# Performance work log

Measured on AMD Instinct MI355X. Metric: run time of the kernel, lower is better.

## Reference

```python
import jax, jax.numpy as jnp
import numpy as np

N_NODES = 50000
N_EDGES = 800000
IN_FEAT = 128
HIDDEN = 256
OUT = 64


def setup_inputs() -> dict:
    key = jax.random.key(0)
    ks = jax.random.split(key, 8)
    x = jax.random.normal(ks[0], (N_NODES, IN_FEAT), dtype=jnp.float32)
    edge_index = jax.random.randint(ks[1], (2, N_EDGES), 0, N_NODES, dtype=jnp.int64)
    s1 = 1.0 / np.sqrt(IN_FEAT)
    s2 = 1.0 / np.sqrt(HIDDEN)
    W1_l = jax.random.uniform(ks[2], (HIDDEN, IN_FEAT), jnp.float32, -s1, s1)
    W1_r = jax.random.uniform(ks[3], (HIDDEN, IN_FEAT), jnp.float32, -s1, s1)
    b1 = jax.random.uniform(ks[4], (HIDDEN,), jnp.float32, -s1, s1)
    W2_l = jax.random.uniform(ks[5], (OUT, HIDDEN), jnp.float32, -s2, s2)
    W2_r = jax.random.uniform(ks[6], (OUT, HIDDEN), jnp.float32, -s2, s2)
    b2 = jax.random.uniform(ks[7], (OUT,), jnp.float32, -s2, s2)
    return {"x": x, "edge_index": edge_index, "W1_l": W1_l, "W1_r": W1_r,
            "b1": b1, "W2_l": W2_l, "W2_r": W2_r, "b2": b2}


def _sage_conv(x, src, dst, W_l, W_r, b):
    # mean aggregation of source features onto destination nodes
    msgs = x[src]                                                   # [E, F]
    agg = jax.ops.segment_sum(msgs, dst, num_segments=N_NODES)      # [N, F]
    cnt = jax.ops.segment_sum(jnp.ones((src.shape[0], 1), x.dtype), dst,
                              num_segments=N_NODES)                 # [N, 1]
    agg = agg / jnp.maximum(cnt, 1.0)
    # out = lin_l(agg) + lin_r(x); bias only on lin_l (PyG SAGEConv)
    return agg @ W_l.T + b + x @ W_r.T


def reference(x, edge_index, W1_l, W1_r, b1, W2_l, W2_r, b2):
    src, dst = edge_index[0], edge_index[1]
    h = jax.nn.relu(_sage_conv(x, src, dst, W1_l, W1_r, b1))
    # dropout is identity in eval mode
    return _sage_conv(h, src, dst, W2_l, W2_r, b2)
```

## Files before the change

kernel.cpp:

```cpp
#include <hip/hip_runtime.h>
#include <hip/hip_bf16.h>

#define N_NODES 50000
#define N_EDGES 800000
#define IN_FEAT 128
#define HIDDEN  256
#define OUT_F   64
#define M_PAD   50048
#define CONV_NB 1024
#define GATH_NB 2048
#define NGROUPS 12500
#define BSH     7
#define NBUCK   391
#define NCHUNK  256
#define BCAP    4096

typedef __attribute__((ext_vector_type(8))) short short8;
typedef __attribute__((ext_vector_type(4))) float f32x4;

static __device__ __forceinline__ unsigned short f2bf(float f) {
    unsigned u = __float_as_uint(f);
    unsigned r = (u + 0x7fffu + ((u >> 16) & 1u)) >> 16;
    return (unsigned short)r;
}
static __device__ __forceinline__ float bflo(unsigned u) { return __uint_as_float(u << 16); }
static __device__ __forceinline__ float bfhi(unsigned u) { return __uint_as_float(u & 0xffff0000u); }

__global__ __launch_bounds__(256) void prep_k(const float* __restrict__ x,
                                              unsigned int* __restrict__ A1u,
                                              const float* __restrict__ W1l,
                                              const float* __restrict__ W1r,
                                              unsigned int* __restrict__ Wf1,
                                              const float* __restrict__ W2l,
                                              const float* __restrict__ W2r,
                                              unsigned int* __restrict__ Wf2,
                                              int* __restrict__ gcur) {
    int b = blockIdx.x, t = threadIdx.x;
    if (b < CONV_NB) {
        const int T = CONV_NB * 256;
        const float4* X4 = (const float4*)x;
        for (int i = b * 256 + t; i < N_NODES * 32; i += T) {
            int n = i >> 5, p4 = i & 31;
            float4 v = X4[i];
            unsigned lo = (unsigned)f2bf(v.x) | ((unsigned)f2bf(v.y) << 16);
            unsigned hi = (unsigned)f2bf(v.z) | ((unsigned)f2bf(v.w) << 16);
            unsigned int* dstp = A1u + (size_t)n * 128 + 64 + p4 * 2;
            dstp[0] = lo; dstp[1] = hi;
        }
    } else if (b < CONV_NB + 128) {
        int i = (b - CONV_NB) * 256 + t;
        int s = i * 2;
        int j = s & 7, lane = (s >> 3) & 63, nt = (s >> 9) & 15, ks = s >> 13;
        int n = nt * 16 + (lane & 15);
        int k = ks * 32 + ((lane >> 4) << 3) + j;
        float v0, v1;
        if (k < 128) { v0 = W1l[n * 128 + k];       v1 = W1l[n * 128 + k + 1]; }
        else         { v0 = W1r[n * 128 + k - 128]; v1 = W1r[n * 128 + k - 127]; }
        Wf1[i] = (unsigned)f2bf(v0) | ((unsigned)f2bf(v1) << 16);
    } else if (b < CONV_NB + 128 + 64) {
        int i = (b - CONV_NB - 128) * 256 + t;
        int s = i * 2;
        int j = s & 7, lane = (s >> 3) & 63, nt = (s >> 9) & 7, ks = s >> 12;
        int n = nt * 16 + (lane & 15);
        int k = ks * 32 + ((lane >> 4) << 3) + j;
        float v0, v1;
        if (n < 64) { v0 = W2l[n * 256 + k];        v1 = W2l[n * 256 + k + 1]; }
        else        { v0 = W2r[(n - 64) * 256 + k]; v1 = W2r[(n - 64) * 256 + k + 1]; }
        Wf2[i] = (unsigned)f2bf(v0) | ((unsigned)f2bf(v1) << 16);
    } else {
        for (int i = t; i < NBUCK; i += 256) gcur[i] = 0;
    }
}

__global__ __launch_bounds__(256) void reorder2_k(const int* __restrict__ dst,
                                                  const int* __restrict__ src,
                                                  int* __restrict__ gcur,
                                                  int2* __restrict__ ebuf) {
    __shared__ int hist[NBUCK];
    __shared__ int cur[NBUCK];
    int b = blockIdx.x, t = threadIdx.x;
    for (int i = t; i < NBUCK; i += 256) hist[i] = 0;
    __syncthreads();
    for (int e = b * 256 + t; e < N_EDGES; e += NCHUNK * 256)
        atomicAdd(&hist[dst[e] >> BSH], 1);
    __syncthreads();
    for (int i = t; i < NBUCK; i += 256) {
        int h = hist[i];
        cur[i] = (h > 0) ? atomicAdd(&gcur[i], h) : 0;
    }
    __syncthreads();
    for (int e = b * 256 + t; e < N_EDGES; e += NCHUNK * 256) {
        int d = dst[e], sv = src[e];
        int q = d >> BSH;
        int pos = atomicAdd(&cur[q], 1);
        if (pos < BCAP) ebuf[(size_t)q * BCAP + pos] = make_int2(sv, d);
    }
}

__global__ __launch_bounds__(256) void bucketcsr_k(const int2* __restrict__ ebuf,
                                                   const int* __restrict__ gcur,
                                                   int* __restrict__ rowptr,
                                                   int* __restrict__ degv,
                                                   int* __restrict__ eids) {
    __shared__ int2 ed[BCAP];
    __shared__ int cnt[128];
    __shared__ int s[256];
    __shared__ int cur[128];
    int b = blockIdx.x, t = threadIdx.x;
    int e0 = b * BCAP;
    int m = gcur[b]; if (m > BCAP) m = BCAP;
    int d0 = b << BSH;
    if (t < 128) cnt[t] = 0;
    for (int i = t; i < m; i += 256) ed[i] = ebuf[e0 + i];
    __syncthreads();
    for (int i = t; i < m; i += 256) atomicAdd(&cnt[ed[i].y - d0], 1);
    __syncthreads();
    s[t] = (t < 128) ? cnt[t] : 0;
    __syncthreads();
    for (int off = 1; off < 256; off <<= 1) {
        int add = (t >= off) ? s[t - off] : 0;
        __syncthreads();
        s[t] += add;
        __syncthreads();
    }
    if (t < 128) {
        int excl = s[t] - cnt[t];
        cur[t] = excl;
        int node = d0 + t;
        if (node < N_NODES) { rowptr[node] = e0 + excl; degv[node] = cnt[t]; }
    }
    __syncthreads();
    for (int i = t; i < m; i += 256) {
        int pos = atomicAdd(&cur[ed[i].y - d0], 1);
        eids[e0 + pos] = ed[i].x;
    }
}

__global__ __launch_bounds__(256) void gather1_k(const unsigned int* __restrict__ Au,
                                                 const int* __restrict__ eids,
                                                 const int* __restrict__ rowptr,
                                                 const int* __restrict__ degv,
                                                 unsigned int* __restrict__ Aw) {
    int w = threadIdx.x >> 6, lane = threadIdx.x & 63;
    int eg = lane >> 4, cq = lane & 15;
    for (int g = blockIdx.x; g < NGROUPS; g += GATH_NB) {
        int node = g * 4 + w;
        int b = rowptr[node], e = b + degv[node];
        float a0 = 0.f, a1 = 0.f, a2 = 0.f, a3 = 0.f, a4 = 0.f, a5 = 0.f, a6 = 0.f, a7 = 0.f;
        int i = b + eg;
        for (; i + 12 < e; i += 16) {
            int s0 = eids[i], s1 = eids[i + 4], s2 = eids[i + 8], s3 = eids[i + 12];
            uint4 v0 = ((const uint4*)(Au + (size_t)s0 * 128 + 64))[cq];
            uint4 v1 = ((const uint4*)(Au + (size_t)s1 * 128 + 64))[cq];
            uint4 v2 = ((const uint4*)(Au + (size_t)s2 * 128 + 64))[cq];
            uint4 v3 = ((const uint4*)(Au + (size_t)s3 * 128 + 64))[cq];
            a0 += bflo(v0.x) + bflo(v1.x) + bflo(v2.x) + bflo(v3.x);
            a1 += bfhi(v0.x) + bfhi(v1.x) + bfhi(v2.x) + bfhi(v3.x);
            a2 += bflo(v0.y) + bflo(v1.y) + bflo(v2.y) + bflo(v3.y);
            a3 += bfhi(v0.y) + bfhi(v1.y) + bfhi(v2.y) + bfhi(v3.y);
            a4 += bflo(v0.z) + bflo(v1.z) + bflo(v2.z) + bflo(v3.z);
            a5 += bfhi(v0.z) + bfhi(v1.z) + bfhi(v2.z) + bfhi(v3.z);
            a6 += bflo(v0.w) + bflo(v1.w) + bflo(v2.w) + bflo(v3.w);
            a7 += bfhi(v0.w) + bfhi(v1.w) + bfhi(v2.w) + bfhi(v3.w);
        }
        for (; i < e; i += 4) {
            int s = eids[i];
            uint4 v = ((const uint4*)(Au + (size_t)s * 128 + 64))[cq];
            a0 += bflo(v.x); a1 += bfhi(v.x);
            a2 += bflo(v.y); a3 += bfhi(v.y);
            a4 += bflo(v.z); a5 += bfhi(v.z);
            a6 += bflo(v.w); a7 += bfhi(v.w);
        }
#pragma unroll
        for (int m = 16; m <= 32; m <<= 1) {
            a0 += __shfl_xor(a0, m); a1 += __shfl_xor(a1, m);
            a2 += __shfl_xor(a2, m); a3 += __shfl_xor(a3, m);
            a4 += __shfl_xor(a4, m); a5 += __shfl_xor(a5, m);
            a6 += __shfl_xor(a6, m); a7 += __shfl_xor(a7, m);
        }
        if (eg == 0) {
            int deg = e - b; if (deg < 1) deg = 1;
            float inv = 1.f / (float)deg;
            uint4 r;
            r.x = (unsigned)f2bf(a0 * inv) | ((unsigned)f2bf(a1 * inv) << 16);
            r.y = (unsigned)f2bf(a2 * inv) | ((unsigned)f2bf(a3 * inv) << 16);
            r.z = (unsigned)f2bf(a4 * inv) | ((unsigned)f2bf(a5 * inv) << 16);
            r.w = (unsigned)f2bf(a6 * inv) | ((unsigned)f2bf(a7 * inv) << 16);
            ((uint4*)(Aw + (size_t)node * 128))[cq] = r;
        }
    }
}

__global__ __launch_bounds__(256) void mfma_gemm1_k(
        const unsigned short* __restrict__ A, const unsigned short* __restrict__ Wf,
        const float* __restrict__ b1, unsigned short* __restrict__ h) {
    int wv = threadIdx.x >> 6, lane = threadIdx.x & 63;
    int rowh = wv >> 1, colh = wv & 1;
    int m0 = blockIdx.x * 64 + rowh * 32;
    int row = lane & 15, kg = lane >> 4;
    const short8* Wf8 = (const short8*)Wf;

    short8 af[2][8];
#pragma unroll
    for (int mt = 0; mt < 2; mt++) {
        const short8* ar = (const short8*)(A + (size_t)(m0 + mt * 16 + row) * 256 + kg * 8);
#pragma unroll
        for (int ks = 0; ks < 8; ks++) af[mt][ks] = ar[ks * 4];
    }
    f32x4 acc[2][8];
#pragma unroll
    for (int mt = 0; mt < 2; mt++)
#pragma unroll
        for (int nt = 0; nt < 8; nt++) acc[mt][nt] = (f32x4)(0.f);

#pragma unroll
    for (int ks = 0; ks < 8; ks++) {
        short8 bf[8];
#pragma unroll
        for (int nt = 0; nt < 8; nt++)
            bf[nt] = Wf8[(ks * 16 + colh * 8 + nt) * 64 + lane];
#pragma unroll
        for (int nt = 0; nt < 8; nt++) {
#pragma unroll
            for (int mt = 0; mt < 2; mt++)
                acc[mt][nt] = __builtin_amdgcn_mfma_f32_16x16x32_bf16(af[mt][ks], bf[nt],
                                                                      acc[mt][nt], 0, 0, 0);
        }
    }

#pragma unroll
    for (int mt = 0; mt < 2; mt++) {
        int r0 = m0 + mt * 16 + kg * 4;
#pragma unroll
        for (int nt = 0; nt < 8; nt++) {
            int c = colh * 128 + nt * 16 + row;
            float bias = b1[c];
#pragma unroll
            for (int i = 0; i < 4; i++) {
                float v = acc[mt][nt][i] + bias;
                v = v > 0.f ? v : 0.f;
                h[(size_t)(r0 + i) * 256 + c] = f2bf(v);
            }
        }
    }
}

__global__ __launch_bounds__(256) void mfma_gemm2_k(
        const unsigned short* __restrict__ A, const unsigned short* __restrict__ Wf,
        const float* __restrict__ b2, unsigned short* __restrict__ y,
        float* __restrict__ out) {
    int wv = threadIdx.x >> 6, lane = threadIdx.x & 63;
    int m0 = blockIdx.x * 128 + wv * 32;
    int row = lane & 15, kg = lane >> 4;
    const short8* Wf8 = (const short8*)Wf;

    short8 af[2][8];
#pragma unroll
    for (int mt = 0; mt < 2; mt++) {
        const short8* ar = (const short8*)(A + (size_t)(m0 + mt * 16 + row) * 256 + kg * 8);
#pragma unroll
        for (int ks = 0; ks < 8; ks++) af[mt][ks] = ar[ks * 4];
    }
    f32x4 acc[2][8];
#pragma unroll
    for (int mt = 0; mt < 2; mt++)
#pragma unroll
        for (int nt = 0; nt < 8; nt++) acc[mt][nt] = (f32x4)(0.f);

#pragma unroll
    for (int ks = 0; ks < 8; ks++) {
        short8 bf[8];
#pragma unroll
        for (int nt = 0; nt < 8; nt++)
            bf[nt] = Wf8[(ks * 8 + nt) * 64 + lane];
#pragma unroll
        for (int nt = 0; nt < 8; nt++) {
#pragma unroll
            for (int mt = 0; mt < 2; mt++)
                acc[mt][nt] = __builtin_amdgcn_mfma_f32_16x16x32_bf16(af[mt][ks], bf[nt],
                                                                      acc[mt][nt], 0, 0, 0);
        }
    }

#pragma unroll
    for (int mt = 0; mt < 2; mt++) {
        int r0 = m0 + mt * 16 + kg * 4;
#pragma unroll
        for (int nt = 0; nt < 8; nt++) {
            int c = nt * 16 + row;
#pragma unroll
            for (int i = 0; i < 4; i++) {
                int rr = r0 + i;
                if (nt < 4) {
                    y[(size_t)rr * OUT_F + c] = f2bf(acc[mt][nt][i]);
                } else if (rr < N_NODES) {
                    out[(size_t)rr * OUT_F + (c - 64)] = acc[mt][nt][i] + b2[c - 64];
                }
            }
        }
    }
}

__global__ __launch_bounds__(256) void gather2_k(const unsigned int* __restrict__ yu,
                                                 const int* __restrict__ eids,
                                                 const int* __restrict__ rowptr,
                                                 const int* __restrict__ degv,
                                                 float* __restrict__ out) {
    int w = threadIdx.x >> 6, lane = threadIdx.x & 63;
    int eg = lane >> 3, cq = lane & 7;
    for (int g = blockIdx.x; g < NGROUPS; g += GATH_NB) {
        int node = g * 4 + w;
        int b = rowptr[node], e = b + degv[node];
        float a0 = 0.f, a1 = 0.f, a2 = 0.f, a3 = 0.f, a4 = 0.f, a5 = 0.f, a6 = 0.f, a7 = 0.f;
        int i = b + eg;
        for (; i + 8 < e; i += 16) {
            int s0 = eids[i], s1 = eids[i + 8];
            uint4 v0 = ((const uint4*)(yu + (size_t)s0 * 32))[cq];
            uint4 v1 = ((const uint4*)(yu + (size_t)s1 * 32))[cq];
            a0 += bflo(v0.x) + bflo(v1.x); a1 += bfhi(v0.x) + bfhi(v1.x);
            a2 += bflo(v0.y) + bflo(v1.y); a3 += bfhi(v0.y) + bfhi(v1.y);
            a4 += bflo(v0.z) + bflo(v1.z); a5 += bfhi(v0.z) + bfhi(v1.z);
            a6 += bflo(v0.w) + bflo(v1.w); a7 += bfhi(v0.w) + bfhi(v1.w);
        }
        for (; i < e; i += 8) {
            int s = eids[i];
            uint4 v = ((const uint4*)(yu + (size_t)s * 32))[cq];
            a0 += bflo(v.x); a1 += bfhi(v.x);
            a2 += bflo(v.y); a3 += bfhi(v.y);
            a4 += bflo(v.z); a5 += bfhi(v.z);
            a6 += bflo(v.w); a7 += bfhi(v.w);
        }
#pragma unroll
        for (int m = 8; m <= 32; m <<= 1) {
            a0 += __shfl_xor(a0, m); a1 += __shfl_xor(a1, m);
            a2 += __shfl_xor(a2, m); a3 += __shfl_xor(a3, m);
            a4 += __shfl_xor(a4, m); a5 += __shfl_xor(a5, m);
            a6 += __shfl_xor(a6, m); a7 += __shfl_xor(a7, m);
        }
        if (eg == 0) {
            int deg = e - b; if (deg < 1) deg = 1;
            float inv = 1.f / (float)deg;
            float4* p = (float4*)(out + (size_t)node * OUT_F + cq * 8);
            float4 c0 = p[0], c1 = p[1];
            c0.x += a0 * inv; c0.y += a1 * inv; c0.z += a2 * inv; c0.w += a3 * inv;
            c1.x += a4 * inv; c1.y += a5 * inv; c1.z += a6 * inv; c1.w += a7 * inv;
            p[0] = c0; p[1] = c1;
        }
    }
}

extern "C" void kernel_launch(void* const* d_in, const int* in_sizes, int n_in,
                              void* d_out, int out_size, void* d_ws, size_t ws_size,
                              hipStream_t stream) {
    const float* x    = (const float*)d_in[0];
    const int*   eidx = (const int*)d_in[1];
    const float* W1l  = (const float*)d_in[2];
    const float* W1r  = (const float*)d_in[3];
    const float* b1   = (const float*)d_in[4];
    const float* W2l  = (const float*)d_in[5];
    const float* W2r  = (const float*)d_in[6];
    const float* b2   = (const float*)d_in[7];
    float* out = (float*)d_out;

    const int* src = eidx;
    const int* dst = eidx + N_EDGES;

    unsigned short* A1   = (unsigned short*)d_ws;
    unsigned short* hbuf = A1 + (size_t)M_PAD * 256;
    unsigned short* ybuf = hbuf + (size_t)M_PAD * 256;
    unsigned short* W1f  = ybuf + (size_t)M_PAD * OUT_F;
    unsigned short* W2f  = W1f + 65536;
    int2* ebuf  = (int2*)(W2f + 32768);
    int* eids   = (int*)(ebuf + (size_t)NBUCK * BCAP);
    int* rowptr = eids + (size_t)NBUCK * BCAP;
    int* degv   = rowptr + N_NODES;
    int* gcur   = degv + N_NODES;

    prep_k<<<CONV_NB + 128 + 64 + 1, 256, 0, stream>>>(x, (unsigned int*)A1,
                                                       W1l, W1r, (unsigned int*)W1f,
                                                       W2l, W2r, (unsigned int*)W2f, gcur);

    reorder2_k<<<NCHUNK, 256, 0, stream>>>(dst, src, gcur, ebuf);

    bucketcsr_k<<<NBUCK, 256, 0, stream>>>(ebuf, gcur, rowptr, degv, eids);

    gather1_k<<<GATH_NB, 256, 0, stream>>>((const unsigned int*)A1, eids, rowptr, degv,
                                           (unsigned int*)A1);

    mfma_gemm1_k<<<M_PAD / 64, 256, 0, stream>>>(A1, W1f, b1, hbuf);

    mfma_gemm2_k<<<M_PAD / 128, 256, 0, stream>>>(hbuf, W2f, b2, ybuf, out);

    gather2_k<<<GATH_NB, 256, 0, stream>>>((const unsigned int*)ybuf, eids, rowptr, degv, out);
}
```

Baseline: 131.6 us.

## Fuse both GEMMs via LDS hidden tile and pack bucket edges into 32-bit

Merges the two MFMA GEMM kernels into one. The ReLU'd hidden activations for a 64-row tile stay in shared memory instead of making a round trip through global memory (about 25 MB of bf16 writes and reads), and one launch is removed. Separately, the bucketed edge buffer now packs the source id and the local destination offset into one int, halving the traffic and LDS use of the CSR build. The packing assumes source ids fit in 16 bits, but there are 50000 nodes (under 65536), so it holds. The fused kernel now needs about 33 KB of LDS per block, which may reduce occupancy.

New measurement: 122.7 us. 1.07x faster.

```diff
diff --git a/kernel.cpp b/kernel.cpp
--- a/kernel.cpp
+++ b/kernel.cpp
@@ -75,7 +75,7 @@
 __global__ __launch_bounds__(256) void reorder2_k(const int* __restrict__ dst,
                                                   const int* __restrict__ src,
                                                   int* __restrict__ gcur,
-                                                  int2* __restrict__ ebuf) {
+                                                  int* __restrict__ ebuf) {
     __shared__ int hist[NBUCK];
     __shared__ int cur[NBUCK];
     int b = blockIdx.x, t = threadIdx.x;
@@ -93,16 +93,16 @@
         int d = dst[e], sv = src[e];
         int q = d >> BSH;
         int pos = atomicAdd(&cur[q], 1);
-        if (pos < BCAP) ebuf[(size_t)q * BCAP + pos] = make_int2(sv, d);
-    }
-}
-
-__global__ __launch_bounds__(256) void bucketcsr_k(const int2* __restrict__ ebuf,
+        if (pos < BCAP) ebuf[(size_t)q * BCAP + pos] = sv | ((d & 127) << 16);
+    }
+}
+
+__global__ __launch_bounds__(256) void bucketcsr_k(const int* __restrict__ ebuf,
                                                    const int* __restrict__ gcur,
                                                    int* __restrict__ rowptr,
                                                    int* __restrict__ degv,
                                                    int* __restrict__ eids) {
-    __shared__ int2 ed[BCAP];
+    __shared__ int ed[BCAP];
     __shared__ int cnt[128];
     __shared__ int s[256];
     __shared__ int cur[128];
@@ -113,7 +113,7 @@
     if (t < 128) cnt[t] = 0;
     for (int i = t; i < m; i += 256) ed[i] = ebuf[e0 + i];
     __syncthreads();
-    for (int i = t; i < m; i += 256) atomicAdd(&cnt[ed[i].y - d0], 1);
+    for (int i = t; i < m; i += 256) atomicAdd(&cnt[ed[i] >> 16], 1);
     __syncthreads();
     s[t] = (t < 128) ? cnt[t] : 0;
     __syncthreads();
@@ -131,8 +131,9 @@
     }
     __syncthreads();
     for (int i = t; i < m; i += 256) {
-        int pos = atomicAdd(&cur[ed[i].y - d0], 1);
-        eids[e0 + pos] = ed[i].x;
+        int v = ed[i];
+        int pos = atomicAdd(&cur[v >> 16], 1);
+        eids[e0 + pos] = v & 0xFFFF;
     }
 }
 
@@ -191,100 +192,85 @@
     }
 }
 
-__global__ __launch_bounds__(256) void mfma_gemm1_k(
-        const unsigned short* __restrict__ A, const unsigned short* __restrict__ Wf,
-        const float* __restrict__ b1, unsigned short* __restrict__ h) {
-    int wv = threadIdx.x >> 6, lane = threadIdx.x & 63;
-    int rowh = wv >> 1, colh = wv & 1;
-    int m0 = blockIdx.x * 64 + rowh * 32;
-    int row = lane & 15, kg = lane >> 4;
-    const short8* Wf8 = (const short8*)Wf;
-
-    short8 af[2][8];
-#pragma unroll
-    for (int mt = 0; mt < 2; mt++) {
-        const short8* ar = (const short8*)(A + (size_t)(m0 + mt * 16 + row) * 256 + kg * 8);
-#pragma unroll
-        for (int ks = 0; ks < 8; ks++) af[mt][ks] = ar[ks * 4];
-    }
-    f32x4 acc[2][8];
-#pragma unroll
-    for (int mt = 0; mt < 2; mt++)
-#pragma unroll
-        for (int nt = 0; nt < 8; nt++) acc[mt][nt] = (f32x4)(0.f);
-
-#pragma unroll
-    for (int ks = 0; ks < 8; ks++) {
-        short8 bf[8];
-#pragma unroll
-        for (int nt = 0; nt < 8; nt++)
-            bf[nt] = Wf8[(ks * 16 + colh * 8 + nt) * 64 + lane];
-#pragma unroll
-        for (int nt = 0; nt < 8; nt++) {
-#pragma unroll
-            for (int mt = 0; mt < 2; mt++)
-                acc[mt][nt] = __builtin_amdgcn_mfma_f32_16x16x32_bf16(af[mt][ks], bf[nt],
-                                                                      acc[mt][nt], 0, 0, 0);
-        }
-    }
-
-#pragma unroll
-    for (int mt = 0; mt < 2; mt++) {
-        int r0 = m0 + mt * 16 + kg * 4;
-#pragma unroll
-        for (int nt = 0; nt < 8; nt++) {
-            int c = colh * 128 + nt * 16 + row;
-            float bias = b1[c];
-#pragma unroll
-            for (int i = 0; i < 4; i++) {
-                float v = acc[mt][nt][i] + bias;
-                v = v > 0.f ? v : 0.f;
-                h[(size_t)(r0 + i) * 256 + c] = f2bf(v);
-            }
-        }
-    }
-}
-
-__global__ __launch_bounds__(256) void mfma_gemm2_k(
-        const unsigned short* __restrict__ A, const unsigned short* __restrict__ Wf,
+__global__ __launch_bounds__(256) void mfma_gemm12_k(
+        const unsigned short* __restrict__ A, const unsigned short* __restrict__ Wf1,
+        const float* __restrict__ b1, const unsigned short* __restrict__ Wf2,
         const float* __restrict__ b2, unsigned short* __restrict__ y,
         float* __restrict__ out) {
+    __shared__ unsigned short hs[64][264];
     int wv = threadIdx.x >> 6, lane = threadIdx.x & 63;
-    int m0 = blockIdx.x * 128 + wv * 32;
     int row = lane & 15, kg = lane >> 4;
-    const short8* Wf8 = (const short8*)Wf;
-
-    short8 af[2][8];
-#pragma unroll
-    for (int mt = 0; mt < 2; mt++) {
-        const short8* ar = (const short8*)(A + (size_t)(m0 + mt * 16 + row) * 256 + kg * 8);
-#pragma unroll
-        for (int ks = 0; ks < 8; ks++) af[mt][ks] = ar[ks * 4];
-    }
-    f32x4 acc[2][8];
-#pragma unroll
-    for (int mt = 0; mt < 2; mt++)
-#pragma unroll
-        for (int nt = 0; nt < 8; nt++) acc[mt][nt] = (f32x4)(0.f);
-
-#pragma unroll
-    for (int ks = 0; ks < 8; ks++) {
-        short8 bf[8];
-#pragma unroll
-        for (int nt = 0; nt < 8; nt++)
-            bf[nt] = Wf8[(ks * 8 + nt) * 64 + lane];
-#pragma unroll
-        for (int nt = 0; nt < 8; nt++) {
-#pragma unroll
-            for (int mt = 0; mt < 2; mt++)
-                acc[mt][nt] = __builtin_amdgcn_mfma_f32_16x16x32_bf16(af[mt][ks], bf[nt],
-                                                                      acc[mt][nt], 0, 0, 0);
-        }
-    }
-
-#pragma unroll
-    for (int mt = 0; mt < 2; mt++) {
-        int r0 = m0 + mt * 16 + kg * 4;
+
+    {
+        int rowh = wv >> 1, colh = wv & 1;
+        int m0 = blockIdx.x * 64 + rowh * 32;
+        const short8* Wf8 = (const short8*)Wf1;
+        short8 af[2][8];
+#pragma unroll
+        for (int mt = 0; mt < 2; mt++) {
+            const short8* ar = (const short8*)(A + (size_t)(m0 + mt * 16 + row) * 256 + kg * 8);
+#pragma unroll
+            for (int ks = 0; ks < 8; ks++) af[mt][ks] = ar[ks * 4];
+        }
+        f32x4 acc[2][8];
+#pragma unroll
+        for (int mt = 0; mt < 2; mt++)
+#pragma unroll
+            for (int nt = 0; nt < 8; nt++) acc[mt][nt] = (f32x4)(0.f);
+#pragma unroll
+        for (int ks = 0; ks < 8; ks++) {
+            short8 bf[8];
+#pragma unroll
+            for (int nt = 0; nt < 8; nt++)
+                bf[nt] = Wf8[(ks * 16 + colh * 8 + nt) * 64 + lane];
+#pragma unroll
+            for (int nt = 0; nt < 8; nt++) {
+#pragma unroll
+                for (int mt = 0; mt < 2; mt++)
+                    acc[mt][nt] = __builtin_amdgcn_mfma_f32_16x16x32_bf16(af[mt][ks], bf[nt],
+                                                                          acc[mt][nt], 0, 0, 0);
+            }
+        }
+#pragma unroll
+        for (int mt = 0; mt < 2; mt++) {
+            int r0l = rowh * 32 + mt * 16 + kg * 4;
+#pragma unroll
+            for (int nt = 0; nt < 8; nt++) {
+                int c = colh * 128 + nt * 16 + row;
+                float bias = b1[c];
+#pragma unroll
+                for (int i = 0; i < 4; i++) {
+                    float v = acc[mt][nt][i] + bias;
+                    v = v > 0.f ? v : 0.f;
+                    hs[r0l + i][c] = f2bf(v);
+                }
+            }
+        }
+    }
+    __syncthreads();
+
+    {
+        int m0l = wv * 16;
+        const short8* Wf8 = (const short8*)Wf2;
+        short8 af2[8];
+#pragma unroll
+        for (int ks = 0; ks < 8; ks++)
+            af2[ks] = *(const short8*)(&hs[m0l + row][kg * 8 + ks * 32]);
+        f32x4 acc2[8];
+#pragma unroll
+        for (int nt = 0; nt < 8; nt++) acc2[nt] = (f32x4)(0.f);
+#pragma unroll
+        for (int ks = 0; ks < 8; ks++) {
+            short8 bf[8];
+#pragma unroll
+            for (int nt = 0; nt < 8; nt++)
+                bf[nt] = Wf8[(ks * 8 + nt) * 64 + lane];
+#pragma unroll
+            for (int nt = 0; nt < 8; nt++)
+                acc2[nt] = __builtin_amdgcn_mfma_f32_16x16x32_bf16(af2[ks], bf[nt],
+                                                                   acc2[nt], 0, 0, 0);
+        }
+        int r0 = blockIdx.x * 64 + m0l + kg * 4;
 #pragma unroll
         for (int nt = 0; nt < 8; nt++) {
             int c = nt * 16 + row;
@@ -292,9 +278,9 @@
             for (int i = 0; i < 4; i++) {
                 int rr = r0 + i;
                 if (nt < 4) {
-                    y[(size_t)rr * OUT_F + c] = f2bf(acc[mt][nt][i]);
+                    y[(size_t)rr * OUT_F + c] = f2bf(acc2[nt][i]);
                 } else if (rr < N_NODES) {
-                    out[(size_t)rr * OUT_F + (c - 64)] = acc[mt][nt][i] + b2[c - 64];
+                    out[(size_t)rr * OUT_F + (c - 64)] = acc2[nt][i] + b2[c - 64];
                 }
             }
         }
@@ -366,12 +352,11 @@
     const int* dst = eidx + N_EDGES;
 
     unsigned short* A1   = (unsigned short*)d_ws;
-    unsigned short* hbuf = A1 + (size_t)M_PAD * 256;
-    unsigned short* ybuf = hbuf + (size_t)M_PAD * 256;
+    unsigned short* ybuf = A1 + (size_t)M_PAD * 256;
     unsigned short* W1f  = ybuf + (size_t)M_PAD * OUT_F;
     unsigned short* W2f  = W1f + 65536;
-    int2* ebuf  = (int2*)(W2f + 32768);
-    int* eids   = (int*)(ebuf + (size_t)NBUCK * BCAP);
+    int* ebuf   = (int*)(W2f + 32768);
+    int* eids   = ebuf + (size_t)NBUCK * BCAP;
     int* rowptr = eids + (size_t)NBUCK * BCAP;
     int* degv   = rowptr + N_NODES;
     int* gcur   = degv + N_NODES;
@@ -387,9 +372,7 @@
     gather1_k<<<GATH_NB, 256, 0, stream>>>((const unsigned int*)A1, eids, rowptr, degv,
                                            (unsigned int*)A1);
 
-    mfma_gemm1_k<<<M_PAD / 64, 256, 0, stream>>>(A1, W1f, b1, hbuf);
-
-    mfma_gemm2_k<<<M_PAD / 128, 256, 0, stream>>>(hbuf, W2f, b2, ybuf, out);
+    mfma_gemm12_k<<<M_PAD / 64, 256, 0, stream>>>(A1, W1f, b1, W2f, b2, ybuf, out);
 
     gather2_k<<<GATH_NB, 256, 0, stream>>>((const unsigned int*)ybuf, eids, rowptr, degv, out);
 }
```
